# Optimization experiments

Measured on AMD Instinct MI355X. Metric: run time of the kernel, lower is better.

## Reference

```python
import jax, jax.numpy as jnp
import numpy as np

N, C, F, E = 32768, 256, 1024, 16
TOP_K = 2


def setup_inputs() -> dict:
    key = jax.random.key(0)
    k_x, k_gw, k_w1, k_w2 = jax.random.split(key, 4)
    x = jax.random.normal(k_x, (N, C), dtype=jnp.float32)
    gate_W = jax.random.normal(k_gw, (E, C), dtype=jnp.float32) * 0.01  # nn.init.normal_(std=0.01)
    gate_b = jnp.zeros((E,), dtype=jnp.float32)
    W1 = jax.random.normal(k_w1, (E, C, F), dtype=jnp.float32) * 0.02
    b1 = jnp.zeros((E, F), dtype=jnp.float32)
    W2 = jax.random.normal(k_w2, (E, F, C), dtype=jnp.float32) * 0.02
    b2 = jnp.zeros((E, C), dtype=jnp.float32)
    return {"x": x, "gate_W": gate_W, "gate_b": gate_b,
            "W1": W1, "b1": b1, "W2": W2, "b2": b2}


def reference(x, gate_W, gate_b, W1, b1, W2, b2):
    # Gating (eval mode: no gaussian noise)
    gate_logits = x @ gate_W.T + gate_b                       # [N, E]
    gate_probs = jax.nn.softmax(gate_logits, axis=-1)
    gate_entropy = -(gate_probs * jnp.log(gate_probs + 1e-8)).sum(axis=-1).mean()

    topk_val, topk_idx = jax.lax.top_k(gate_logits, TOP_K)   # [N, K]
    gate_weights = jax.nn.softmax(topk_val, axis=-1)          # softmax over the top-k logits

    # Dense all-expert FFN compute (matches the torch stack over experts)
    h = jax.nn.relu(jnp.einsum('nc,ecf->enf', x, W1) + b1[:, None, :])   # [E, N, F]
    expert_outputs = jnp.einsum('enf,efc->enc', h, W2) + b2[:, None, :]  # [E, N, C]

    # Gather top-k expert outputs per token and combine
    eo = jnp.transpose(expert_outputs, (1, 0, 2))             # [N, E, C]
    selected = jnp.take_along_axis(eo, topk_idx[:, :, None], axis=1)  # [N, K, C]
    out = (gate_weights[:, :, None] * selected).sum(axis=1)  # [N, C]

    # default args: return_gate=False, return_entropy=True
    return out, gate_entropy
```

## Files before the change

kernel.cpp:

```cpp
#include <hip/hip_runtime.h>
#include <hip/hip_bf16.h>
#include <math.h>

#define N_TOK 32768
#define C_DIM 256
#define F_DIM 1024
#define E_NUM 16
#define TILE_R 128
#define NCH 16

typedef unsigned short u16;
typedef unsigned int u32;
typedef __attribute__((ext_vector_type(4))) u16 u16x4;
typedef __attribute__((ext_vector_type(8))) u16 u16x8;
typedef __attribute__((ext_vector_type(8))) short bf16x8;
typedef __attribute__((ext_vector_type(4))) u32 u32x4;
typedef __attribute__((ext_vector_type(16))) float f32x16;

#define AS1 __attribute__((address_space(1)))
#define AS3 __attribute__((address_space(3)))

__device__ __forceinline__ void gload16(const void* g, void* lds) {
    __builtin_amdgcn_global_load_lds((const AS1 u32*)(uintptr_t)g,
                                     (AS3 u32*)(u32)(uintptr_t)lds, 16, 0, 0);
}

__device__ __forceinline__ u16 f2bf(float f) {
    union { float f; u32 u; } v; v.f = f;
    u32 r = v.u + 0x7fffu + ((v.u >> 16) & 1u);
    return (u16)(r >> 16);
}


__global__ __launch_bounds__(256) void gate_kernel(
    const float* __restrict__ x, const float* __restrict__ gW,
    const float* __restrict__ gb, float* __restrict__ ent_out,
    int* __restrict__ tidx, float* __restrict__ tw, int* __restrict__ counts,
    u16* __restrict__ xb)
{
    __shared__ float gws[E_NUM * C_DIM];
    __shared__ float gbs[E_NUM];
    __shared__ float went[4];
    __shared__ int lc[E_NUM];
    int tid = threadIdx.x;

    for (int i = tid; i < E_NUM * C_DIM / 4; i += 256)
        ((float4*)gws)[i] = ((const float4*)gW)[i];
    if (tid < E_NUM) { gbs[tid] = gb[tid]; lc[tid] = 0; }
    __syncthreads();

    int tok = tid >> 2, q = tid & 3;
    int n = blockIdx.x * 64 + tok;
    const float* xr = x + (size_t)n * C_DIM;

    float4 xv[16];
    #pragma unroll
    for (int j = 0; j < 16; j++)
        xv[j] = *(const float4*)(xr + j * 16 + q * 4);

    #pragma unroll
    for (int j = 0; j < 16; j++) {
        u16x4 o;
        o[0] = f2bf(xv[j].x); o[1] = f2bf(xv[j].y);
        o[2] = f2bf(xv[j].z); o[3] = f2bf(xv[j].w);
        *(u16x4*)(xb + (size_t)n * C_DIM + j * 16 + q * 4) = o;
    }

    float lg[E_NUM];
    #pragma unroll
    for (int e = 0; e < E_NUM; e++) lg[e] = 0.f;
    #pragma unroll
    for (int j = 0; j < 16; j++) {
        #pragma unroll
        for (int e = 0; e < E_NUM; e++) {
            float4 g = *(const float4*)(gws + e * C_DIM + j * 16 + q * 4);
            lg[e] += xv[j].x * g.x + xv[j].y * g.y + xv[j].z * g.z + xv[j].w * g.w;
        }
    }
    #pragma unroll
    for (int e = 0; e < E_NUM; e++) {
        lg[e] += __shfl_xor(lg[e], 1);
        lg[e] += __shfl_xor(lg[e], 2);
        lg[e] += gbs[e];
    }

    float m = lg[0];
    #pragma unroll
    for (int e = 1; e < E_NUM; e++) m = fmaxf(m, lg[e]);
    float s = 0.f, ex[E_NUM];
    #pragma unroll
    for (int e = 0; e < E_NUM; e++) { ex[e] = __expf(lg[e] - m); s += ex[e]; }
    float inv = 1.f / s;
    float ent = 0.f;
    #pragma unroll
    for (int e = 0; e < E_NUM; e++) {
        float p = ex[e] * inv;
        ent -= p * logf(p + 1e-8f);
    }

    float v0 = -1e30f, v1 = -1e30f;
    int i0 = 0, i1 = 0;
    #pragma unroll
    for (int e = 0; e < E_NUM; e++) {
        float l = lg[e];
        if (l > v0) { v1 = v0; i1 = i0; v0 = l; i0 = e; }
        else if (l > v1) { v1 = l; i1 = e; }
    }
    if (q == 0) {
        float w1e = __expf(v1 - v0);
        float z = 1.f + w1e;
        tidx[2 * n] = i0; tidx[2 * n + 1] = i1;
        tw[2 * n] = 1.f / z; tw[2 * n + 1] = w1e / z;
        atomicAdd(&lc[i0], 1);
        atomicAdd(&lc[i1], 1);
    }

    float v = ent;
    for (int off = 32; off > 0; off >>= 1) v += __shfl_down(v, off);
    int wid = tid >> 6, lane = tid & 63;
    if (lane == 0) went[wid] = v;
    __syncthreads();
    if (tid == 0)
        atomicAdd(ent_out, (went[0] + went[1] + went[2] + went[3]) * (1.0f / (4.0f * N_TOK)));
    if (tid < E_NUM && lc[tid]) atomicAdd(&counts[tid], lc[tid]);
}

__global__ void prefix_kernel(const int* __restrict__ counts,
                              int* __restrict__ offs, int* __restrict__ tp)
{
    if (threadIdx.x == 0 && blockIdx.x == 0) {
        int o = 0, t = 0;
        offs[0] = 0; tp[0] = 0;
        for (int e = 0; e < E_NUM; e++) {
            o += counts[e];
            t += (counts[e] + TILE_R - 1) / TILE_R;
            offs[e + 1] = o;
            tp[e + 1] = t;
        }
    }
}

__global__ __launch_bounds__(256) void scatter_kernel(
    const int* __restrict__ tidx, const float* __restrict__ tw,
    const int* __restrict__ offs, int* __restrict__ fill,
    int* __restrict__ tok, float* __restrict__ wgt, int* __restrict__ pairpos)
{
    __shared__ int lc[E_NUM], lbase[E_NUM];
    int tid = threadIdx.x;
    if (tid < E_NUM) lc[tid] = 0;
    __syncthreads();
    int n = blockIdx.x * 256 + tid;
    int e0 = tidx[2 * n], e1 = tidx[2 * n + 1];
    int r0 = atomicAdd(&lc[e0], 1);
    int r1 = atomicAdd(&lc[e1], 1);
    __syncthreads();
    if (tid < E_NUM) lbase[tid] = offs[tid] + atomicAdd(&fill[tid], lc[tid]);
    __syncthreads();
    int p0 = lbase[e0] + r0, p1 = lbase[e1] + r1;
    tok[p0] = n; wgt[p0] = tw[2 * n];     pairpos[2 * n] = p0;
    tok[p1] = n; wgt[p1] = tw[2 * n + 1]; pairpos[2 * n + 1] = p1;
}

__global__ __launch_bounds__(256) void tcvt_kernel(
    const float* __restrict__ src, u16* __restrict__ dst, int R, int Cc)
{
    __shared__ float t[64][65];
    int e = blockIdx.x;
    int r0 = blockIdx.y << 6, c0 = blockIdx.z << 6;
    const float* s = src + (size_t)e * R * Cc;
    u16* d = dst + (size_t)e * R * Cc;
    int tid = threadIdx.x;
    int rr = tid >> 4, cc = (tid & 15) << 2;
    #pragma unroll
    for (int it = 0; it < 4; it++) {
        float4 v = *(const float4*)(s + (size_t)(r0 + rr + it * 16) * Cc + c0 + cc);
        t[rr + it * 16][cc] = v.x; t[rr + it * 16][cc + 1] = v.y;
        t[rr + it * 16][cc + 2] = v.z; t[rr + it * 16][cc + 3] = v.w;
    }
    __syncthreads();
    int cr = tid >> 3, rq = (tid & 7) << 3;
    #pragma unroll
    for (int it = 0; it < 2; it++) {
        int c = cr + it * 32;
        u16x8 o;
        #pragma unroll
        for (int j = 0; j < 8; j++) o[j] = f2bf(t[rq + j][c]);
        *(u16x8*)(d + (size_t)(c0 + c) * R + r0 + rq) = o;
    }
}

#define HS_OFF  131072
#define B1S_OFF 147456

template <int MODE>
__global__ __launch_bounds__(512, 2) void ffn_mfma(
    const u16* __restrict__ xb, const u16* __restrict__ w1t,
    const u16* __restrict__ w2t, const float* __restrict__ b1,
    const float* __restrict__ b2, const int* __restrict__ tok,
    const float* __restrict__ wgt, const int* __restrict__ offs,
    const int* __restrict__ tp, float* __restrict__ ybuf,
    float* __restrict__ out)
{
    __shared__ __align__(1024) char smem[152576];
    int* s_tok = (int*)(smem + 151552);
    float* s_w = (float*)(smem + 152064);
    float* b1s = (float*)(smem + B1S_OFF);

    int b = blockIdx.x;
    if (b >= tp[E_NUM]) return;
    int e = 0;
    while (b >= tp[e + 1]) e++;
    int base = offs[e] + ((b - tp[e]) << 7);
    int rows = offs[e + 1] - base; if (rows > TILE_R) rows = TILE_R;

    int tid = threadIdx.x;
    int lane = tid & 63, wid = tid >> 6;
    int hi = lane >> 5;
    int wr = wid >> 1, wc = wid & 1;

    const u16* w1e = w1t + (size_t)e * (F_DIM * C_DIM);
    const u16* w2e = w2t + (size_t)e * (C_DIM * F_DIM);
    const float* b1e = b1 + e * F_DIM;
    const float* b2e = b2 + e * C_DIM;

    if (tid < TILE_R) {
        int src = (tid < rows) ? base + tid : base;
        s_tok[tid] = tok[src];
        s_w[tid] = (tid < rows) ? wgt[src] : 0.f;
    }
    if (tid < 256) ((float4*)b1s)[tid] = ((const float4*)b1e)[tid];
    __syncthreads();

    #pragma unroll
    for (int i = 0; i < 8; i++) {
        int idx = (wid << 3) + i;
        int row = ((idx >> 4) << 5) + (lane & 31);
        gload16(xb + ((size_t)s_tok[row] << 8) + ((idx & 15) << 4) + (hi << 3),
                smem + (idx << 10));
    }
    __syncthreads();

    bf16x8 xr[16];
    #pragma unroll
    for (int ks = 0; ks < 16; ks++)
        xr[ks] = *(const bf16x8*)(smem + (wr << 14) + (ks << 10) + (lane << 4));
    __syncthreads();

    u32x4 sg[8];
    #pragma unroll
    for (int i = 0; i < 4; i++) {
        int idx = (wid << 2) + i;
        int f = ((idx >> 4) << 5) + (lane & 31);
        sg[i] = *(const u32x4*)(w1e + ((size_t)f << 8) + ((idx & 15) << 4) + (hi << 3));
        int c = ((idx >> 2) << 5) + (lane & 31);
        sg[4 + i] = *(const u32x4*)(w2e + ((size_t)c << 10) + ((idx & 3) << 4) + (hi << 3));
    }
    #pragma unroll
    for (int i = 0; i < 4; i++) {
        int idx = (wid << 2) + i;
        *(u32x4*)(smem + (idx << 10) + (lane << 4)) = sg[i];
        *(u32x4*)(smem + 32768 + (idx << 10) + (lane << 4)) = sg[4 + i];
    }

    f32x16 acc2[4];
    #pragma unroll
    for (int ct = 0; ct < 4; ct++) acc2[ct] = (f32x16)(0.0f);

    for (int ch = 0; ch < NCH; ch++) {
        int cur = ch & 1;
        const char* cbuf = smem + (cur << 16);

        asm volatile("s_waitcnt lgkmcnt(0)" ::: "memory");
        __builtin_amdgcn_s_barrier();
        __builtin_amdgcn_sched_barrier(0);

        {
            int chn = ch + 1; if (chn == NCH) chn = NCH - 1;
            #pragma unroll
            for (int i = 0; i < 4; i++) {
                int idx = (wid << 2) + i;
                int f = (chn << 6) + ((idx >> 4) << 5) + (lane & 31);
                sg[i] = *(const u32x4*)(w1e + ((size_t)f << 8) + ((idx & 15) << 4) + (hi << 3));
                int c = ((idx >> 2) << 5) + (lane & 31);
                sg[4 + i] = *(const u32x4*)(w2e + ((size_t)c << 10) + (chn << 6) + ((idx & 3) << 4) + (hi << 3));
            }
        }

        const char* w1b = cbuf + (wc << 14) + (lane << 4);
        f32x16 acc1 = (f32x16)(0.0f);
        __builtin_amdgcn_s_setprio(1);
        #pragma unroll
        for (int ks = 0; ks < 16; ks++) {
            bf16x8 a = *(const bf16x8*)(w1b + (ks << 10));
            acc1 = __builtin_amdgcn_mfma_f32_32x32x16_bf16(a, xr[ks], acc1, 0, 0, 0);
        }
        __builtin_amdgcn_s_setprio(0);

        float h[16];
        #pragma unroll
        for (int r = 0; r < 16; r++) {
            int fl = (wc << 5) + (r & 3) + ((r >> 2) << 3) + (hi << 2);
            h[r] = fmaxf(acc1[r] + b1s[(ch << 6) + fl], 0.f);
        }
        u32 w[8];
        #pragma unroll
        for (int t = 0; t < 8; t++)
            asm("v_cvt_pk_bf16_f32 %0, %1, %2" : "=v"(w[t]) : "v"(h[2 * t]), "v"(h[2 * t + 1]));
        asm volatile("v_permlane32_swap_b32 %0, %1" : "+v"(w[0]), "+v"(w[2]));
        asm volatile("v_permlane32_swap_b32 %0, %1" : "+v"(w[1]), "+v"(w[3]));
        asm volatile("v_permlane32_swap_b32 %0, %1" : "+v"(w[4]), "+v"(w[6]));
        asm volatile("v_permlane32_swap_b32 %0, %1" : "+v"(w[5]), "+v"(w[7]));
        union { u32x4 u; bf16x8 v; } fr0, fr1, pr0, pr1;
        fr0.u = (u32x4){w[0], w[1], w[2], w[3]};
        fr1.u = (u32x4){w[4], w[5], w[6], w[7]};

        *(u32x4*)(smem + HS_OFF + (wr << 12) + ((wc << 1) << 10) + (lane << 4)) = fr0.u;
        *(u32x4*)(smem + HS_OFF + (wr << 12) + (((wc << 1) + 1) << 10) + (lane << 4)) = fr1.u;

        asm volatile("s_waitcnt lgkmcnt(0)" ::: "memory");
        __builtin_amdgcn_s_barrier();
        __builtin_amdgcn_sched_barrier(0);

        {
            char* nbuf = smem + ((cur ^ 1) << 16);
            #pragma unroll
            for (int i = 0; i < 4; i++) {
                int idx = (wid << 2) + i;
                *(u32x4*)(nbuf + (idx << 10) + (lane << 4)) = sg[i];
                *(u32x4*)(nbuf + 32768 + (idx << 10) + (lane << 4)) = sg[4 + i];
            }
        }

        pr0.u = *(const u32x4*)(smem + HS_OFF + (wr << 12) + (((wc ^ 1) << 1) << 10) + (lane << 4));
        pr1.u = *(const u32x4*)(smem + HS_OFF + (wr << 12) + ((((wc ^ 1) << 1) + 1) << 10) + (lane << 4));

        const char* w2b = cbuf + 32768 + (wc << 14) + (lane << 4);
        bf16x8 bh0, bh1, bh2, bh3;
        if (wc == 0) { bh0 = fr0.v; bh1 = fr1.v; bh2 = pr0.v; bh3 = pr1.v; }
        else         { bh0 = pr0.v; bh1 = pr1.v; bh2 = fr0.v; bh3 = fr1.v; }

        __builtin_amdgcn_s_setprio(1);
        #define P2_STEP(BH, S2)                                               \
            _Pragma("unroll")                                                 \
            for (int ctl = 0; ctl < 4; ctl++) {                               \
                bf16x8 a = *(const bf16x8*)(w2b + (ctl << 12) + ((S2) << 10));\
                acc2[ctl] = __builtin_amdgcn_mfma_f32_32x32x16_bf16(a, BH, acc2[ctl], 0, 0, 0); \
            }
        P2_STEP(bh0, 0)
        P2_STEP(bh1, 1)
        P2_STEP(bh2, 2)
        P2_STEP(bh3, 3)
        #undef P2_STEP
        __builtin_amdgcn_s_setprio(0);
    }

    int m = (wr << 5) + (lane & 31);
    if (m < rows) {
        if (MODE == 0) {
            float* yr = ybuf + ((size_t)(base + m) << 8) + (wc << 7);
            #pragma unroll
            for (int ctl = 0; ctl < 4; ctl++) {
                #pragma unroll
                for (int rq = 0; rq < 4; rq++) {
                    int c = (ctl << 5) + (rq << 3) + (hi << 2);
                    float4 v = {acc2[ctl][4 * rq],     acc2[ctl][4 * rq + 1],
                                acc2[ctl][4 * rq + 2], acc2[ctl][4 * rq + 3]};
                    *(float4*)(yr + c) = v;
                }
            }
        } else {
            float wgt_m = s_w[m];
            float* orow = out + ((size_t)s_tok[m] << 8) + (wc << 7);
            const float* b2w = b2e + (wc << 7);
            #pragma unroll
            for (int ctl = 0; ctl < 4; ctl++) {
                #pragma unroll
                for (int rq = 0; rq < 4; rq++) {
                    int c = (ctl << 5) + (rq << 3) + (hi << 2);
                    #pragma unroll
                    for (int l = 0; l < 4; l++)
                        atomicAdd(&orow[c + l],
                                  wgt_m * (acc2[ctl][4 * rq + l] + b2w[c + l]));
                }
            }
        }
    }
}

__global__ __launch_bounds__(256) void combine_kernel(
    const float* __restrict__ ybuf, const int* __restrict__ tidx,
    const float* __restrict__ tw, const int* __restrict__ pairpos,
    const float* __restrict__ b2, float* __restrict__ out)
{
    int idx = blockIdx.x * 256 + threadIdx.x;
    int n = idx >> 6;
    int q = (idx & 63) << 2;
    int e0 = tidx[2 * n], e1 = tidx[2 * n + 1];
    float w0 = tw[2 * n], w1 = tw[2 * n + 1];
    int p0 = pairpos[2 * n], p1 = pairpos[2 * n + 1];
    float4 y0 = *(const float4*)(ybuf + ((size_t)p0 << 8) + q);
    float4 y1 = *(const float4*)(ybuf + ((size_t)p1 << 8) + q);
    float4 c0 = *(const float4*)(b2 + (e0 << 8) + q);
    float4 c1 = *(const float4*)(b2 + (e1 << 8) + q);
    float4 o;
    o.x = w0 * (y0.x + c0.x) + w1 * (y1.x + c1.x);
    o.y = w0 * (y0.y + c0.y) + w1 * (y1.y + c1.y);
    o.z = w0 * (y0.z + c0.z) + w1 * (y1.z + c1.z);
    o.w = w0 * (y0.w + c0.w) + w1 * (y1.w + c1.w);
    *(float4*)(out + ((size_t)n << 8) + q) = o;
}

extern "C" void kernel_launch(void* const* d_in, const int* in_sizes, int n_in,
                              void* d_out, int out_size, void* d_ws, size_t ws_size,
                              hipStream_t stream)
{
    const float* x   = (const float*)d_in[0];
    const float* gW  = (const float*)d_in[1];
    const float* gb  = (const float*)d_in[2];
    const float* W1  = (const float*)d_in[3];
    const float* b1  = (const float*)d_in[4];
    const float* W2  = (const float*)d_in[5];
    const float* b2  = (const float*)d_in[6];
    float* out = (float*)d_out;

    char* ws = (char*)d_ws;
    int*   topk_idx = (int*)(ws + 0);
    float* topk_w   = (float*)(ws + 262144);
    int*   tok      = (int*)(ws + 524288);
    float* wgt      = (float*)(ws + 786432);
    int*   pairpos  = (int*)(ws + 1048576);
    int*   counts   = (int*)(ws + 1310720);
    int*   fill     = (int*)(ws + 1310784);
    int*   offs     = (int*)(ws + 1310848);
    int*   tp       = (int*)(ws + 1310916);

    const size_t XB_OFF  = 2097152;
    const size_t W1T_OFF = 18874368;
    const size_t W2T_OFF = 27262976;
    const size_t Y_OFF   = 35651584;
    const size_t WS_FULL = Y_OFF + (size_t)2 * N_TOK * C_DIM * 4;

    u16* xb  = (u16*)(ws + XB_OFF);
    u16* w1t = (u16*)(ws + W1T_OFF);
    u16* w2t = (u16*)(ws + W2T_OFF);
    float* ybuf = (float*)(ws + Y_OFF);

    int mode = (ws_size >= WS_FULL) ? 0 : 1;

    hipMemsetAsync(d_out, 0, (size_t)(N_TOK * C_DIM + 1) * sizeof(float), stream);
    hipMemsetAsync(counts, 0, 2 * E_NUM * sizeof(int), stream);

    float* ent_out = out + (size_t)N_TOK * C_DIM;

    gate_kernel<<<N_TOK / 64, 256, 0, stream>>>(x, gW, gb, ent_out,
                                                topk_idx, topk_w, counts, xb);
    prefix_kernel<<<1, 64, 0, stream>>>(counts, offs, tp);
    scatter_kernel<<<N_TOK / 256, 256, 0, stream>>>(topk_idx, topk_w, offs,
                                                    fill, tok, wgt, pairpos);
    tcvt_kernel<<<dim3(E_NUM, C_DIM / 64, F_DIM / 64), 256, 0, stream>>>(W1, w1t, C_DIM, F_DIM);
    tcvt_kernel<<<dim3(E_NUM, F_DIM / 64, C_DIM / 64), 256, 0, stream>>>(W2, w2t, F_DIM, C_DIM);

    if (mode == 0) {
        ffn_mfma<0><<<544, 512, 0, stream>>>(xb, w1t, w2t, b1, b2, tok, wgt,
                                             offs, tp, ybuf, out);
        combine_kernel<<<N_TOK * 64 / 256, 256, 0, stream>>>(ybuf, topk_idx,
                                                             topk_w, pairpos, b2, out);
    } else {
        ffn_mfma<1><<<544, 512, 0, stream>>>(xb, w1t, w2t, b1, b2, tok, wgt,
                                             offs, tp, ybuf, out);
    }
}
```

Baseline: 222.2 us.

## Store expert outputs in bf16, remap blocks, split MFMA accumulators, trim memset

The intermediate per-pair expert output buffer is stored as bf16 instead of fp32, halving its write and read traffic between the FFN and combine kernels. Block indices are remapped with an 8-way stride, probably to spread each expert's blocks across XCDs. The first GEMM's 16-step MFMA chain is split across two independent accumulators to shorten the dependency chain. The full output memset is skipped in the combine path, leaving only the entropy scalar cleared. The cost is extra rounding of the expert outputs to bf16 before combining.

```diff
diff --git a/kernel.cpp b/kernel.cpp
--- a/kernel.cpp
+++ b/kernel.cpp
@@ -8,6 +8,7 @@
 #define E_NUM 16
 #define TILE_R 128
 #define NCH 16
+#define NBLK 544
 
 typedef unsigned short u16;
 typedef unsigned int u32;
@@ -29,6 +30,11 @@
     union { float f; u32 u; } v; v.f = f;
     u32 r = v.u + 0x7fffu + ((v.u >> 16) & 1u);
     return (u16)(r >> 16);
+}
+
+__device__ __forceinline__ float bf2f(u16 b) {
+    union { u32 u; float f; } v; v.u = ((u32)b) << 16;
+    return v.f;
 }
 
 
@@ -198,7 +204,7 @@
     const u16* __restrict__ w2t, const float* __restrict__ b1,
     const float* __restrict__ b2, const int* __restrict__ tok,
     const float* __restrict__ wgt, const int* __restrict__ offs,
-    const int* __restrict__ tp, float* __restrict__ ybuf,
+    const int* __restrict__ tp, u16* __restrict__ ybuf,
     float* __restrict__ out)
 {
     __shared__ __align__(1024) char smem[152576];
@@ -206,7 +212,8 @@
     float* s_w = (float*)(smem + 152064);
     float* b1s = (float*)(smem + B1S_OFF);
 
-    int b = blockIdx.x;
+    int idx = blockIdx.x;
+    int b = (idx & 7) * (NBLK / 8) + (idx >> 3);
     if (b >= tp[E_NUM]) return;
     int e = 0;
     while (b >= tp[e + 1]) e++;
@@ -233,10 +240,10 @@
 
     #pragma unroll
     for (int i = 0; i < 8; i++) {
-        int idx = (wid << 3) + i;
-        int row = ((idx >> 4) << 5) + (lane & 31);
-        gload16(xb + ((size_t)s_tok[row] << 8) + ((idx & 15) << 4) + (hi << 3),
-                smem + (idx << 10));
+        int idx2 = (wid << 3) + i;
+        int row = ((idx2 >> 4) << 5) + (lane & 31);
+        gload16(xb + ((size_t)s_tok[row] << 8) + ((idx2 & 15) << 4) + (hi << 3),
+                smem + (idx2 << 10));
     }
     __syncthreads();
 
@@ -249,17 +256,17 @@
     u32x4 sg[8];
     #pragma unroll
     for (int i = 0; i < 4; i++) {
-        int idx = (wid << 2) + i;
-        int f = ((idx >> 4) << 5) + (lane & 31);
-        sg[i] = *(const u32x4*)(w1e + ((size_t)f << 8) + ((idx & 15) << 4) + (hi << 3));
-        int c = ((idx >> 2) << 5) + (lane & 31);
-        sg[4 + i] = *(const u32x4*)(w2e + ((size_t)c << 10) + ((idx & 3) << 4) + (hi << 3));
+        int idx2 = (wid << 2) + i;
+        int f = ((idx2 >> 4) << 5) + (lane & 31);
+        sg[i] = *(const u32x4*)(w1e + ((size_t)f << 8) + ((idx2 & 15) << 4) + (hi << 3));
+        int c = ((idx2 >> 2) << 5) + (lane & 31);
+        sg[4 + i] = *(const u32x4*)(w2e + ((size_t)c << 10) + ((idx2 & 3) << 4) + (hi << 3));
     }
     #pragma unroll
     for (int i = 0; i < 4; i++) {
-        int idx = (wid << 2) + i;
-        *(u32x4*)(smem + (idx << 10) + (lane << 4)) = sg[i];
-        *(u32x4*)(smem + 32768 + (idx << 10) + (lane << 4)) = sg[4 + i];
+        int idx2 = (wid << 2) + i;
+        *(u32x4*)(smem + (idx2 << 10) + (lane << 4)) = sg[i];
+        *(u32x4*)(smem + 32768 + (idx2 << 10) + (lane << 4)) = sg[4 + i];
     }
 
     f32x16 acc2[4];
@@ -278,21 +285,23 @@
             int chn = ch + 1; if (chn == NCH) chn = NCH - 1;
             #pragma unroll
             for (int i = 0; i < 4; i++) {
-                int idx = (wid << 2) + i;
-                int f = (chn << 6) + ((idx >> 4) << 5) + (lane & 31);
-                sg[i] = *(const u32x4*)(w1e + ((size_t)f << 8) + ((idx & 15) << 4) + (hi << 3));
-                int c = ((idx >> 2) << 5) + (lane & 31);
-                sg[4 + i] = *(const u32x4*)(w2e + ((size_t)c << 10) + (chn << 6) + ((idx & 3) << 4) + (hi << 3));
+                int idx2 = (wid << 2) + i;
+                int f = (chn << 6) + ((idx2 >> 4) << 5) + (lane & 31);
+                sg[i] = *(const u32x4*)(w1e + ((size_t)f << 8) + ((idx2 & 15) << 4) + (hi << 3));
+                int c = ((idx2 >> 2) << 5) + (lane & 31);
+                sg[4 + i] = *(const u32x4*)(w2e + ((size_t)c << 10) + (chn << 6) + ((idx2 & 3) << 4) + (hi << 3));
             }
         }
 
         const char* w1b = cbuf + (wc << 14) + (lane << 4);
-        f32x16 acc1 = (f32x16)(0.0f);
+        f32x16 acc1a = (f32x16)(0.0f), acc1b = (f32x16)(0.0f);
         __builtin_amdgcn_s_setprio(1);
         #pragma unroll
-        for (int ks = 0; ks < 16; ks++) {
-            bf16x8 a = *(const bf16x8*)(w1b + (ks << 10));
-            acc1 = __builtin_amdgcn_mfma_f32_32x32x16_bf16(a, xr[ks], acc1, 0, 0, 0);
+        for (int ks = 0; ks < 8; ks++) {
+            bf16x8 a0 = *(const bf16x8*)(w1b + ((2 * ks) << 10));
+            bf16x8 a1 = *(const bf16x8*)(w1b + ((2 * ks + 1) << 10));
+            acc1a = __builtin_amdgcn_mfma_f32_32x32x16_bf16(a0, xr[2 * ks], acc1a, 0, 0, 0);
+            acc1b = __builtin_amdgcn_mfma_f32_32x32x16_bf16(a1, xr[2 * ks + 1], acc1b, 0, 0, 0);
         }
         __builtin_amdgcn_s_setprio(0);
 
@@ -300,7 +309,7 @@
         #pragma unroll
         for (int r = 0; r < 16; r++) {
             int fl = (wc << 5) + (r & 3) + ((r >> 2) << 3) + (hi << 2);
-            h[r] = fmaxf(acc1[r] + b1s[(ch << 6) + fl], 0.f);
+            h[r] = fmaxf(acc1a[r] + acc1b[r] + b1s[(ch << 6) + fl], 0.f);
         }
         u32 w[8];
         #pragma unroll
@@ -325,9 +334,9 @@
             char* nbuf = smem + ((cur ^ 1) << 16);
             #pragma unroll
             for (int i = 0; i < 4; i++) {
-                int idx = (wid << 2) + i;
-                *(u32x4*)(nbuf + (idx << 10) + (lane << 4)) = sg[i];
-                *(u32x4*)(nbuf + 32768 + (idx << 10) + (lane << 4)) = sg[4 + i];
+                int idx2 = (wid << 2) + i;
+                *(u32x4*)(nbuf + (idx2 << 10) + (lane << 4)) = sg[i];
+                *(u32x4*)(nbuf + 32768 + (idx2 << 10) + (lane << 4)) = sg[4 + i];
             }
         }
 
@@ -357,15 +366,18 @@
     int m = (wr << 5) + (lane & 31);
     if (m < rows) {
         if (MODE == 0) {
-            float* yr = ybuf + ((size_t)(base + m) << 8) + (wc << 7);
+            u16* yr = ybuf + ((size_t)(base + m) << 8) + (wc << 7);
             #pragma unroll
             for (int ctl = 0; ctl < 4; ctl++) {
                 #pragma unroll
                 for (int rq = 0; rq < 4; rq++) {
                     int c = (ctl << 5) + (rq << 3) + (hi << 2);
-                    float4 v = {acc2[ctl][4 * rq],     acc2[ctl][4 * rq + 1],
-                                acc2[ctl][4 * rq + 2], acc2[ctl][4 * rq + 3]};
-                    *(float4*)(yr + c) = v;
+                    u16x4 o;
+                    o[0] = f2bf(acc2[ctl][4 * rq]);
+                    o[1] = f2bf(acc2[ctl][4 * rq + 1]);
+                    o[2] = f2bf(acc2[ctl][4 * rq + 2]);
+                    o[3] = f2bf(acc2[ctl][4 * rq + 3]);
+                    *(u16x4*)(yr + c) = o;
                 }
             }
         } else {
@@ -388,7 +400,7 @@
 }
 
 __global__ __launch_bounds__(256) void combine_kernel(
-    const float* __restrict__ ybuf, const int* __restrict__ tidx,
+    const u16* __restrict__ ybuf, const int* __restrict__ tidx,
     const float* __restrict__ tw, const int* __restrict__ pairpos,
     const float* __restrict__ b2, float* __restrict__ out)
 {
@@ -398,15 +410,15 @@
     int e0 = tidx[2 * n], e1 = tidx[2 * n + 1];
     float w0 = tw[2 * n], w1 = tw[2 * n + 1];
     int p0 = pairpos[2 * n], p1 = pairpos[2 * n + 1];
-    float4 y0 = *(const float4*)(ybuf + ((size_t)p0 << 8) + q);
-    float4 y1 = *(const float4*)(ybuf + ((size_t)p1 << 8) + q);
+    u16x4 y0 = *(const u16x4*)(ybuf + ((size_t)p0 << 8) + q);
+    u16x4 y1 = *(const u16x4*)(ybuf + ((size_t)p1 << 8) + q);
     float4 c0 = *(const float4*)(b2 + (e0 << 8) + q);
     float4 c1 = *(const float4*)(b2 + (e1 << 8) + q);
     float4 o;
-    o.x = w0 * (y0.x + c0.x) + w1 * (y1.x + c1.x);
-    o.y = w0 * (y0.y + c0.y) + w1 * (y1.y + c1.y);
-    o.z = w0 * (y0.z + c0.z) + w1 * (y1.z + c1.z);
-    o.w = w0 * (y0.w + c0.w) + w1 * (y1.w + c1.w);
+    o.x = w0 * (bf2f(y0[0]) + c0.x) + w1 * (bf2f(y1[0]) + c1.x);
+    o.y = w0 * (bf2f(y0[1]) + c0.y) + w1 * (bf2f(y1[1]) + c1.y);
+    o.z = w0 * (bf2f(y0[2]) + c0.z) + w1 * (bf2f(y1[2]) + c1.z);
+    o.w = w0 * (bf2f(y0[3]) + c0.w) + w1 * (bf2f(y1[3]) + c1.w);
     *(float4*)(out + ((size_t)n << 8) + q) = o;
 }
 
@@ -438,19 +450,23 @@
     const size_t W1T_OFF = 18874368;
     const size_t W2T_OFF = 27262976;
     const size_t Y_OFF   = 35651584;
-    const size_t WS_FULL = Y_OFF + (size_t)2 * N_TOK * C_DIM * 4;
+    const size_t WS_FULL = Y_OFF + (size_t)2 * N_TOK * C_DIM * 2;
 
     u16* xb  = (u16*)(ws + XB_OFF);
     u16* w1t = (u16*)(ws + W1T_OFF);
     u16* w2t = (u16*)(ws + W2T_OFF);
-    float* ybuf = (float*)(ws + Y_OFF);
+    u16* ybuf = (u16*)(ws + Y_OFF);
 
     int mode = (ws_size >= WS_FULL) ? 0 : 1;
 
-    hipMemsetAsync(d_out, 0, (size_t)(N_TOK * C_DIM + 1) * sizeof(float), stream);
+    float* ent_out = out + (size_t)N_TOK * C_DIM;
+
+    if (mode == 0) {
+        hipMemsetAsync(ent_out, 0, sizeof(float), stream);
+    } else {
+        hipMemsetAsync(d_out, 0, (size_t)(N_TOK * C_DIM + 1) * sizeof(float), stream);
+    }
     hipMemsetAsync(counts, 0, 2 * E_NUM * sizeof(int), stream);
-
-    float* ent_out = out + (size_t)N_TOK * C_DIM;
 
     gate_kernel<<<N_TOK / 64, 256, 0, stream>>>(x, gW, gb, ent_out,
                                                 topk_idx, topk_w, counts, xb);
@@ -461,12 +477,12 @@
     tcvt_kernel<<<dim3(E_NUM, F_DIM / 64, C_DIM / 64), 256, 0, stream>>>(W2, w2t, F_DIM, C_DIM);
 
     if (mode == 0) {
-        ffn_mfma<0><<<544, 512, 0, stream>>>(xb, w1t, w2t, b1, b2, tok, wgt,
-                                             offs, tp, ybuf, out);
+        ffn_mfma<0><<<NBLK, 512, 0, stream>>>(xb, w1t, w2t, b1, b2, tok, wgt,
+                                              offs, tp, ybuf, out);
         combine_kernel<<<N_TOK * 64 / 256, 256, 0, stream>>>(ybuf, topk_idx,
                                                              topk_w, pairpos, b2, out);
     } else {
-        ffn_mfma<1><<<544, 512, 0, stream>>>(xb, w1t, w2t, b1, b2, tok, wgt,
-                                             offs, tp, ybuf, out);
-    }
-}
+        ffn_mfma<1><<<NBLK, 512, 0, stream>>>(xb, w1t, w2t, b1, b2, tok, wgt,
+                                              offs, tp, ybuf, out);
+    }
+}
```

Measured after the change: 212.2 us. 1.05x faster.
